# Kernel tuning notes

Measured on AMD Instinct MI355X. Metric: run time of the kernel, lower is better.

## Reference

```python
import jax, jax.numpy as jnp
import numpy as np

B, S, D, H = 4, 2048, 512, 8
DH = D // H  # 64


def setup_inputs() -> dict:
    key = jax.random.key(0)
    ks = jax.random.split(key, 12)
    sc = 0.02
    return {
        "embed": jax.random.normal(ks[0], (B, S, D), dtype=jnp.float32),
        "Wq": jax.random.normal(ks[1], (H, DH, D), dtype=jnp.float32) * sc,
        "bq": jax.random.normal(ks[2], (H, DH), dtype=jnp.float32) * sc,
        "Wk": jax.random.normal(ks[3], (H, DH, D), dtype=jnp.float32) * sc,
        "bk": jax.random.normal(ks[4], (H, DH), dtype=jnp.float32) * sc,
        "Wv": jax.random.normal(ks[5], (H, DH, D), dtype=jnp.float32) * sc,
        "bv": jax.random.normal(ks[6], (H, DH), dtype=jnp.float32) * sc,
        "Wo": jax.random.normal(ks[7], (D, D), dtype=jnp.float32) * sc,
        "bo": jax.random.normal(ks[8], (D,), dtype=jnp.float32) * sc,
        "gamma": jnp.ones((D,), dtype=jnp.float32),
        "beta": jnp.zeros((D,), dtype=jnp.float32),
    }


def reference(embed, Wq, bq, Wk, bk, Wv, bv, Wo, bo, gamma, beta):
    # Per-head linear projections, vectorized over heads: [B,H,S,DH]
    q = jnp.einsum("bsd,hed->bhse", embed, Wq) + bq[None, :, None, :]
    k = jnp.einsum("bsd,hed->bhse", embed, Wk) + bk[None, :, None, :]
    v = jnp.einsum("bsd,hed->bhse", embed, Wv) + bv[None, :, None, :]

    # Full score matrix [B,H,S,S], tril applied to RAW scores (zeros, not -inf),
    # scaled by sqrt(embedding_dim) -- faithful to the original module's math.
    att = jnp.einsum("bhse,bhte->bhst", q, k)
    att = jnp.tril(att)
    att = att / jnp.sqrt(jnp.float32(D))
    att = jax.nn.softmax(att, axis=-1)

    out = jnp.einsum("bhst,bhte->bhse", att, v)  # [B,H,S,DH]
    # concat heads along feature dim -> [B,S,D]
    out = jnp.transpose(out, (0, 2, 1, 3)).reshape(B, S, D)

    x = out @ Wo.T + bo
    x = x + embed

    # LayerNorm over last dim
    mu = jnp.mean(x, axis=-1, keepdims=True)
    var = jnp.var(x, axis=-1, keepdims=True)
    x = (x - mu) / jnp.sqrt(var + 1e-5) * gamma + beta
    return x
```

## Files before the change

kernel.cpp:

```cpp
#include <hip/hip_runtime.h>
#include <hip/hip_bf16.h>


typedef __bf16 bf16;
typedef __bf16 bf16x8 __attribute__((ext_vector_type(8)));
typedef __bf16 bf16x4v __attribute__((ext_vector_type(4)));
typedef float f32x4 __attribute__((ext_vector_type(4)));

#define S_LEN 2048
#define DMODEL 512
#define QSCALE 0.06375870914f

#define GLDS(g, l) __builtin_amdgcn_global_load_lds(                  \
    (const __attribute__((address_space(1))) void*)(g),               \
    (__attribute__((address_space(3))) void*)(l), 16, 0, 0)

__global__ __launch_bounds__(256) void cast_f32_bf16(const float* __restrict__ in,
                                                     bf16* __restrict__ out, int n4) {
  int i = blockIdx.x * blockDim.x + threadIdx.x;
  if (i < n4) {
    float4 v = reinterpret_cast<const float4*>(in)[i];
    bf16x4v o;
    o[0] = (bf16)v.x; o[1] = (bf16)v.y; o[2] = (bf16)v.z; o[3] = (bf16)v.w;
    *reinterpret_cast<bf16x4v*>(out + (size_t)i * 4) = o;
  }
}

__global__ __launch_bounds__(256) void cast4_f32_bf16(
    const float* __restrict__ a0, const float* __restrict__ a1,
    const float* __restrict__ a2, const float* __restrict__ a3,
    bf16* __restrict__ o0, bf16* __restrict__ o1,
    bf16* __restrict__ o2, bf16* __restrict__ o3) {
  int y = blockIdx.y;
  const float* in = (y == 0) ? a0 : (y == 1) ? a1 : (y == 2) ? a2 : a3;
  bf16* out = (y == 0) ? o0 : (y == 1) ? o1 : (y == 2) ? o2 : o3;
  int i = blockIdx.x * blockDim.x + threadIdx.x;
  float4 v = reinterpret_cast<const float4*>(in)[i];
  bf16x4v o;
  o[0] = (bf16)v.x; o[1] = (bf16)v.y; o[2] = (bf16)v.z; o[3] = (bf16)v.w;
  *reinterpret_cast<bf16x4v*>(out + (size_t)i * 4) = o;
}

__device__ __forceinline__ void gemm128_core(
    const bf16* __restrict__ A, const bf16* __restrict__ Bw,
    int row0, int col0, bf16* As, bf16* Bs, f32x4 (&acc)[4][4]) {
  int tid = threadIdx.x;
  int w = tid >> 6, l = tid & 63, lr = l & 15, lg = l >> 4;
  int wr = w >> 1, wc = w & 1;

  int srow = w * 8 + (l >> 3);
  int scol = ((l & 7) ^ (srow & 7)) << 3;
  const bf16* ga = A + (size_t)(row0 + srow) * DMODEL + scol;
  const bf16* gb = Bw + (size_t)(col0 + srow) * DMODEL + scol;
  char* asb = (char*)As;
  char* bsb = (char*)Bs;
  int sbase = w * 1024;

  int aoff[4], boff[4];
#pragma unroll
  for (int m = 0; m < 4; ++m) {
    aoff[m] = (wr * 64 + m * 16 + lr) * 128 + (((lg ^ (lr & 7))) << 4);
    boff[m] = (wc * 64 + m * 16 + lr) * 128 + (((lg ^ (lr & 7))) << 4);
  }

  for (int k0 = 0; k0 < DMODEL; k0 += 64) {
#pragma unroll
    for (int qt = 0; qt < 4; ++qt) {
      GLDS(ga + (size_t)qt * 32 * DMODEL, asb + qt * 4096 + sbase);
      GLDS(gb + (size_t)qt * 32 * DMODEL, bsb + qt * 4096 + sbase);
    }
    ga += 64; gb += 64;
    __syncthreads();

    bf16x8 af[2][4], bfv[2][4];
#pragma unroll
    for (int m = 0; m < 4; ++m) {
      af[0][m] = *(const bf16x8*)(asb + aoff[m]);
      af[1][m] = *(const bf16x8*)(asb + (aoff[m] ^ 0x40));
      bfv[0][m] = *(const bf16x8*)(bsb + boff[m]);
      bfv[1][m] = *(const bf16x8*)(bsb + (boff[m] ^ 0x40));
    }
#pragma unroll
    for (int m = 0; m < 4; ++m)
#pragma unroll
      for (int n = 0; n < 4; ++n) {
        acc[m][n] = __builtin_amdgcn_mfma_f32_16x16x32_bf16(af[0][m], bfv[0][n], acc[m][n], 0, 0, 0);
        acc[m][n] = __builtin_amdgcn_mfma_f32_16x16x32_bf16(af[1][m], bfv[1][n], acc[m][n], 0, 0, 0);
      }
    __syncthreads();
  }
}

__global__ __launch_bounds__(256) void gemm_qkv(
    const bf16* __restrict__ A, const bf16* __restrict__ Wqkv,
    const float* __restrict__ bq, const float* __restrict__ bk, const float* __restrict__ bv,
    bf16* __restrict__ Qb, bf16* __restrict__ Kb, bf16* __restrict__ Vt) {
  __shared__ __align__(16) bf16 As[128 * 64];
  __shared__ __align__(16) bf16 Bs[128 * 64];
  int row0 = blockIdx.x * 128, col0 = blockIdx.y * 128;
  f32x4 acc[4][4] = {};
  gemm128_core(A, Wqkv, row0, col0, As, Bs, acc);

  int tid = threadIdx.x;
  int w = tid >> 6, l = tid & 63, lr = l & 15, lg = l >> 4;
  int wr = w >> 1, wc = w & 1;
  int z2 = col0 >> 9;
  if (z2 < 2) {
    bf16* O = z2 ? Kb : Qb;
    const float* bias = z2 ? bk : bq;
    float qs = z2 ? 1.0f : QSCALE;
#pragma unroll
    for (int n = 0; n < 4; ++n) {
      int cg = (col0 & 511) + wc * 64 + n * 16 + lr;
      float bi = bias[cg];
#pragma unroll
      for (int m = 0; m < 4; ++m) {
        int rg = row0 + wr * 64 + m * 16 + lg * 4;
#pragma unroll
        for (int r = 0; r < 4; ++r)
          O[(size_t)(rg + r) * DMODEL + cg] = (bf16)((acc[m][n][r] + bi) * qs);
      }
    }
  } else {
#pragma unroll
    for (int n = 0; n < 4; ++n) {
      int ep = (col0 & 511) + wc * 64 + n * 16 + lr;
      int h = ep >> 6, e = ep & 63;
      float bi = bv[ep];
#pragma unroll
      for (int m = 0; m < 4; ++m) {
        int rg = row0 + wr * 64 + m * 16 + lg * 4;
        int b = rg >> 11, s0 = rg & 2047;
        bf16x4v pk;
#pragma unroll
        for (int r = 0; r < 4; ++r) pk[r] = (bf16)(acc[m][n][r] + bi);
        *(bf16x4v*)(Vt + ((size_t)((b * 8 + h) * 64 + e)) * S_LEN + s0) = pk;
      }
    }
  }
}

__global__ __launch_bounds__(256) void gemm_wo(
    const bf16* __restrict__ A, const bf16* __restrict__ W,
    const float* __restrict__ bo, const float* __restrict__ embed,
    float* __restrict__ X) {
  __shared__ __align__(16) bf16 As[128 * 64];
  __shared__ __align__(16) bf16 Bs[128 * 64];
  int row0 = blockIdx.x * 128, col0 = blockIdx.y * 128;
  f32x4 acc[4][4] = {};
  gemm128_core(A, W, row0, col0, As, Bs, acc);

  int tid = threadIdx.x;
  int w = tid >> 6, l = tid & 63, lr = l & 15, lg = l >> 4;
  int wr = w >> 1, wc = w & 1;
#pragma unroll
  for (int n = 0; n < 4; ++n) {
    int cg = col0 + wc * 64 + n * 16 + lr;
    float bi = bo[cg];
#pragma unroll
    for (int m = 0; m < 4; ++m) {
      int rg = row0 + wr * 64 + m * 16 + lg * 4;
#pragma unroll
      for (int r = 0; r < 4; ++r)
        X[(size_t)(rg + r) * DMODEL + cg] =
            acc[m][n][r] + bi + embed[(size_t)(rg + r) * DMODEL + cg];
    }
  }
}

__global__ __launch_bounds__(256) void suf_kernel(const bf16* __restrict__ Vt,
                                                  float* __restrict__ SUF) {
  int bh = blockIdx.x;
  int e = threadIdx.x & 63;
  int seg = threadIdx.x >> 6;
  __shared__ float segtot[4][64];
  const bf16* vrow = Vt + ((size_t)bh * 64 + e) * S_LEN;
  float loc[32];
  float carry = 0.f;
#pragma unroll
  for (int j = 31; j >= 0; --j) {
    int jj = seg * 32 + j;
    bf16x8 a = *(const bf16x8*)(vrow + jj * 16);
    bf16x8 b2 = *(const bf16x8*)(vrow + jj * 16 + 8);
    float s = 0.f;
#pragma unroll
    for (int k = 0; k < 8; ++k) s += (float)a[k] + (float)b2[k];
    carry += s;
    loc[j] = carry;
  }
  segtot[seg][e] = carry;
  __syncthreads();
  float add = 0.f;
  for (int s2 = seg + 1; s2 < 4; ++s2) add += segtot[s2][e];
  float* srow = SUF + (size_t)bh * 129 * 64 + e;
#pragma unroll
  for (int j = 0; j < 32; ++j) srow[(size_t)(seg * 32 + j) * 64] = loc[j] + add;
  if (threadIdx.x < 64) srow[(size_t)128 * 64] = 0.f;
}

__global__ __launch_bounds__(512) void flash_attn(
    const bf16* __restrict__ Qb, const bf16* __restrict__ Kb,
    const bf16* __restrict__ Vt, const float* __restrict__ SUF,
    bf16* __restrict__ attO) {
  int bh = blockIdx.y;
  int b = bh >> 3, h = bh & 7;
  int p = (int)gridDim.x - 1 - (int)blockIdx.x;
  int tid = threadIdx.x;
  int w = tid >> 6, l = tid & 63, lr = l & 15, lg = l >> 4;
  int wsub = w & 3;
  int qtile = (w < 4) ? (16 + p) : (15 - p);
  int qb = qtile * 64;
  int nt = 17 + p;

  __shared__ __align__(16) bf16 kl[2][64 * 64];
  __shared__ __align__(16) bf16 vl[2][64 * 64];
  __shared__ __align__(16) bf16 pl[8][16 * 64];

  int srow = qb + 16 * wsub + lr;
  const bf16* qptr = Qb + ((size_t)(b * S_LEN) + srow) * DMODEL + h * 64 + lg * 8;
  bf16x8 aq0 = *(const bf16x8*)(qptr);
  bf16x8 aq1 = *(const bf16x8*)(qptr + 32);

  float lsum[4] = {0.f, 0.f, 0.f, 0.f};
  f32x4 acc[4] = {};

  int tmax_w = qb + 16 * wsub + 16;

  int grow = tid >> 3, gch = tid & 7;
  int sch = ((gch ^ (grow & 7)) << 3);
  const bf16* Kg = Kb + ((size_t)(b * S_LEN) + grow) * DMODEL + h * 64 + sch;
  const bf16* Vg = Vt + ((size_t)(bh * 64) + grow) * S_LEN + sch;
  int sdst = w * 1024;

  int sw0 = (lg ^ (lr & 7)) << 4;
  int sw4 = sw0 ^ 0x40;
  char* plb = (char*)pl[w];

  GLDS(Kg, (char*)kl[0] + sdst);
  GLDS(Vg, (char*)vl[0] + sdst);
  asm volatile("s_waitcnt vmcnt(0)" ::: "memory");
  __syncthreads();

  int cur = 0;
  for (int it = 0; it < nt; ++it) {
    int t0 = it << 6;
    if (it + 1 < nt) {
      GLDS(Kg + (size_t)(t0 + 64) * DMODEL, (char*)kl[cur ^ 1] + sdst);
      GLDS(Vg + (t0 + 64), (char*)vl[cur ^ 1] + sdst);
    }
    if (t0 < tmax_w) {
      char* klb = (char*)kl[cur];
      char* vlb = (char*)vl[cur];

      f32x4 sfrag[4];
      const f32x4 fz = {0.f, 0.f, 0.f, 0.f};
#pragma unroll
      for (int c = 0; c < 4; ++c) {
        int rb = (16 * c + lr) * 128;
        bf16x8 bk0 = *(const bf16x8*)(klb + rb + sw0);
        bf16x8 bk1 = *(const bf16x8*)(klb + rb + sw4);
        f32x4 t = __builtin_amdgcn_mfma_f32_16x16x32_bf16(aq0, bk0, fz, 0, 0, 0);
        sfrag[c] = __builtin_amdgcn_mfma_f32_16x16x32_bf16(aq1, bk1, t, 0, 0, 0);
      }

      if (t0 + 64 <= qb + 16 * wsub) {
#pragma unroll
        for (int r = 0; r < 4; ++r) {
          int row = lg * 4 + r;
          int pbase = row * 128 + ((lr & 7) << 1);
          int xorv = row & 7;
          float psum = 0.f;
#pragma unroll
          for (int c = 0; c < 4; ++c) {
            float pv = exp2f(sfrag[c][r]);
            psum += pv;
            int chunk = 2 * c + (lr >> 3);
            *(bf16*)(plb + pbase + (((chunk ^ xorv) << 4))) = (bf16)pv;
          }
          lsum[r] += psum;
        }
      } else {
#pragma unroll
        for (int r = 0; r < 4; ++r) {
          int sg = qb + 16 * wsub + lg * 4 + r;
          int row = lg * 4 + r;
          int pbase = row * 128 + ((lr & 7) << 1);
          int xorv = row & 7;
          float psum = 0.f;
#pragma unroll
          for (int c = 0; c < 4; ++c) {
            int tg = t0 + 16 * c + lr;
            float x = (tg <= sg) ? sfrag[c][r] : ((tg < tmax_w) ? 0.f : -1e30f);
            float pv = exp2f(x);
            psum += pv;
            int chunk = 2 * c + (lr >> 3);
            *(bf16*)(plb + pbase + (((chunk ^ xorv) << 4))) = (bf16)pv;
          }
          lsum[r] += psum;
        }
      }

      bf16x8 pa0 = *(const bf16x8*)(plb + lr * 128 + sw0);
      bf16x8 pa1 = *(const bf16x8*)(plb + lr * 128 + sw4);
#pragma unroll
      for (int c = 0; c < 4; ++c) {
        int rb = (16 * c + lr) * 128;
        bf16x8 bv0 = *(const bf16x8*)(vlb + rb + sw0);
        bf16x8 bv1 = *(const bf16x8*)(vlb + rb + sw4);
        acc[c] = __builtin_amdgcn_mfma_f32_16x16x32_bf16(pa0, bv0, acc[c], 0, 0, 0);
        acc[c] = __builtin_amdgcn_mfma_f32_16x16x32_bf16(pa1, bv1, acc[c], 0, 0, 0);
      }
    }
    asm volatile("s_waitcnt vmcnt(0)" ::: "memory");
    __syncthreads();
    cur ^= 1;
  }

#pragma unroll
  for (int r = 0; r < 4; ++r) {
#pragma unroll
    for (int d = 1; d < 16; d <<= 1) lsum[r] += __shfl_xor(lsum[r], d, 64);
  }

  int j16 = tmax_w >> 4;
  const float* suf = SUF + ((size_t)bh * 129 + j16) * 64;
  float cnt = (float)(S_LEN - tmax_w);
  float sufe[4];
#pragma unroll
  for (int c = 0; c < 4; ++c) sufe[c] = suf[16 * c + lr];
#pragma unroll
  for (int r = 0; r < 4; ++r) {
    float inv = 1.f / (lsum[r] + cnt);
    int sg = qb + 16 * wsub + lg * 4 + r;
#pragma unroll
    for (int c = 0; c < 4; ++c) {
      float o = (acc[c][r] + sufe[c]) * inv;
      attO[((size_t)(b * S_LEN) + sg) * DMODEL + h * 64 + 16 * c + lr] = (bf16)o;
    }
  }
}

__global__ __launch_bounds__(256) void ln_kernel(const float* __restrict__ x,
                                                 const float* __restrict__ gamma,
                                                 const float* __restrict__ beta,
                                                 float* __restrict__ out) {
  int row = blockIdx.x * 4 + (threadIdx.x >> 6);
  int l = threadIdx.x & 63;
  const float4* xr = reinterpret_cast<const float4*>(x + (size_t)row * DMODEL) + l * 2;
  float4 v0 = xr[0], v1 = xr[1];
  float s = v0.x + v0.y + v0.z + v0.w + v1.x + v1.y + v1.z + v1.w;
  float s2 = v0.x * v0.x + v0.y * v0.y + v0.z * v0.z + v0.w * v0.w +
             v1.x * v1.x + v1.y * v1.y + v1.z * v1.z + v1.w * v1.w;
#pragma unroll
  for (int d = 1; d < 64; d <<= 1) {
    s += __shfl_xor(s, d, 64);
    s2 += __shfl_xor(s2, d, 64);
  }
  float mean = s * (1.f / 512.f);
  float var = s2 * (1.f / 512.f) - mean * mean;
  float rstd = rsqrtf(var + 1e-5f);
  const float4* g4 = reinterpret_cast<const float4*>(gamma) + l * 2;
  const float4* b4 = reinterpret_cast<const float4*>(beta) + l * 2;
  float4 g0 = g4[0], g1 = g4[1], bb0 = b4[0], bb1 = b4[1];
  float4 o0, o1;
  o0.x = (v0.x - mean) * rstd * g0.x + bb0.x;
  o0.y = (v0.y - mean) * rstd * g0.y + bb0.y;
  o0.z = (v0.z - mean) * rstd * g0.z + bb0.z;
  o0.w = (v0.w - mean) * rstd * g0.w + bb0.w;
  o1.x = (v1.x - mean) * rstd * g1.x + bb1.x;
  o1.y = (v1.y - mean) * rstd * g1.y + bb1.y;
  o1.z = (v1.z - mean) * rstd * g1.z + bb1.z;
  o1.w = (v1.w - mean) * rstd * g1.w + bb1.w;
  float4* orow = reinterpret_cast<float4*>(out + (size_t)row * DMODEL) + l * 2;
  orow[0] = o0;
  orow[1] = o1;
}

extern "C" void kernel_launch(void* const* d_in, const int* in_sizes, int n_in,
                              void* d_out, int out_size, void* d_ws, size_t ws_size,
                              hipStream_t stream) {
  const float* embed = (const float*)d_in[0];
  const float* Wq = (const float*)d_in[1];
  const float* bq = (const float*)d_in[2];
  const float* Wk = (const float*)d_in[3];
  const float* bk = (const float*)d_in[4];
  const float* Wv = (const float*)d_in[5];
  const float* bv = (const float*)d_in[6];
  const float* Wo = (const float*)d_in[7];
  const float* bo = (const float*)d_in[8];
  const float* gamma = (const float*)d_in[9];
  const float* beta = (const float*)d_in[10];
  float* out = (float*)d_out;

  char* ws = (char*)d_ws;
  size_t off = 0;
  auto alc = [&](size_t b) { size_t o = off; off += (b + 255) & ~(size_t)255; return o; };
  bf16* Eb    = (bf16*)(ws + alc(8192ull * 512 * 2));
  bf16* Wqkv  = (bf16*)(ws + alc(1536ull * 512 * 2));
  bf16* Wob   = (bf16*)(ws + alc(512ull * 512 * 2));
  bf16* Qb    = (bf16*)(ws + alc(8192ull * 512 * 2));
  bf16* Kb    = (bf16*)(ws + alc(8192ull * 512 * 2));
  bf16* Vt    = (bf16*)(ws + alc(8192ull * 512 * 2));
  float* SUF  = (float*)(ws + alc(32ull * 129 * 64 * 4));
  bf16* AttO  = (bf16*)(ws + alc(8192ull * 512 * 2));
  float* Xb   = (float*)(ws + alc(8192ull * 512 * 4));
  (void)ws_size; (void)n_in; (void)in_sizes; (void)out_size;

  cast_f32_bf16<<<4096, 256, 0, stream>>>(embed, Eb, 4194304 / 4);
  cast4_f32_bf16<<<dim3(256, 4), 256, 0, stream>>>(
      Wq, Wk, Wv, Wo, Wqkv, Wqkv + 512ull * 512, Wqkv + 1024ull * 512, Wob);

  gemm_qkv<<<dim3(64, 12), 256, 0, stream>>>(Eb, Wqkv, bq, bk, bv, Qb, Kb, Vt);
  suf_kernel<<<32, 256, 0, stream>>>(Vt, SUF);
  flash_attn<<<dim3(16, 32), 512, 0, stream>>>(Qb, Kb, Vt, SUF, AttO);
  gemm_wo<<<dim3(64, 4), 256, 0, stream>>>(AttO, Wob, bo, embed, Xb);
  ln_kernel<<<2048, 256, 0, stream>>>(Xb, gamma, beta, out);
}
```

Before: 113.9 us.

## Merge cast kernels, store residual in bf16, widen suffix scan, add MFMA priority

Merges the two cast kernels into one launch, stores the Wo-GEMM plus residual output as bf16 instead of fp32 so the LayerNorm reads half the bytes, and splits the suffix-sum kernel across 8 segments with 512 threads. It also raises wave priority around the MFMA blocks in flash attention. The bf16 intermediate loses precision before LayerNorm. The ideas aim to cut launch overhead and memory traffic in the small kernels.

```diff
diff --git a/kernel.cpp b/kernel.cpp
--- a/kernel.cpp
+++ b/kernel.cpp
@@ -15,30 +15,28 @@
     (const __attribute__((address_space(1))) void*)(g),               \
     (__attribute__((address_space(3))) void*)(l), 16, 0, 0)
 
-__global__ __launch_bounds__(256) void cast_f32_bf16(const float* __restrict__ in,
-                                                     bf16* __restrict__ out, int n4) {
-  int i = blockIdx.x * blockDim.x + threadIdx.x;
-  if (i < n4) {
-    float4 v = reinterpret_cast<const float4*>(in)[i];
-    bf16x4v o;
-    o[0] = (bf16)v.x; o[1] = (bf16)v.y; o[2] = (bf16)v.z; o[3] = (bf16)v.w;
-    *reinterpret_cast<bf16x4v*>(out + (size_t)i * 4) = o;
-  }
-}
-
-__global__ __launch_bounds__(256) void cast4_f32_bf16(
-    const float* __restrict__ a0, const float* __restrict__ a1,
-    const float* __restrict__ a2, const float* __restrict__ a3,
-    bf16* __restrict__ o0, bf16* __restrict__ o1,
-    bf16* __restrict__ o2, bf16* __restrict__ o3) {
-  int y = blockIdx.y;
-  const float* in = (y == 0) ? a0 : (y == 1) ? a1 : (y == 2) ? a2 : a3;
-  bf16* out = (y == 0) ? o0 : (y == 1) ? o1 : (y == 2) ? o2 : o3;
-  int i = blockIdx.x * blockDim.x + threadIdx.x;
-  float4 v = reinterpret_cast<const float4*>(in)[i];
+__global__ __launch_bounds__(256) void cast_all(
+    const float* __restrict__ embed, const float* __restrict__ Wq,
+    const float* __restrict__ Wk, const float* __restrict__ Wv,
+    const float* __restrict__ Wo,
+    bf16* __restrict__ Eb, bf16* __restrict__ Wqkv, bf16* __restrict__ Wob) {
+  int i = blockIdx.x * 256 + threadIdx.x;
+  const float* src;
+  bf16* dst;
+  int il;
+  if (i < 1048576) {
+    src = embed; dst = Eb; il = i;
+  } else {
+    int j = i - 1048576;
+    int w = j >> 16;
+    il = j & 65535;
+    src = (w == 0) ? Wq : (w == 1) ? Wk : (w == 2) ? Wv : Wo;
+    dst = (w == 3) ? Wob : Wqkv + (size_t)w * 262144;
+  }
+  float4 v = reinterpret_cast<const float4*>(src)[il];
   bf16x4v o;
   o[0] = (bf16)v.x; o[1] = (bf16)v.y; o[2] = (bf16)v.z; o[3] = (bf16)v.w;
-  *reinterpret_cast<bf16x4v*>(out + (size_t)i * 4) = o;
+  *reinterpret_cast<bf16x4v*>(dst + (size_t)il * 4) = o;
 }
 
 __device__ __forceinline__ void gemm128_core(
@@ -143,7 +141,7 @@
 __global__ __launch_bounds__(256) void gemm_wo(
     const bf16* __restrict__ A, const bf16* __restrict__ W,
     const float* __restrict__ bo, const float* __restrict__ embed,
-    float* __restrict__ X) {
+    bf16* __restrict__ X) {
   __shared__ __align__(16) bf16 As[128 * 64];
   __shared__ __align__(16) bf16 Bs[128 * 64];
   int row0 = blockIdx.x * 128, col0 = blockIdx.y * 128;
@@ -163,23 +161,23 @@
 #pragma unroll
       for (int r = 0; r < 4; ++r)
         X[(size_t)(rg + r) * DMODEL + cg] =
-            acc[m][n][r] + bi + embed[(size_t)(rg + r) * DMODEL + cg];
-    }
-  }
-}
-
-__global__ __launch_bounds__(256) void suf_kernel(const bf16* __restrict__ Vt,
+            (bf16)(acc[m][n][r] + bi + embed[(size_t)(rg + r) * DMODEL + cg]);
+    }
+  }
+}
+
+__global__ __launch_bounds__(512) void suf_kernel(const bf16* __restrict__ Vt,
                                                   float* __restrict__ SUF) {
   int bh = blockIdx.x;
   int e = threadIdx.x & 63;
   int seg = threadIdx.x >> 6;
-  __shared__ float segtot[4][64];
+  __shared__ float segtot[8][64];
   const bf16* vrow = Vt + ((size_t)bh * 64 + e) * S_LEN;
-  float loc[32];
+  float loc[16];
   float carry = 0.f;
 #pragma unroll
-  for (int j = 31; j >= 0; --j) {
-    int jj = seg * 32 + j;
+  for (int j = 15; j >= 0; --j) {
+    int jj = seg * 16 + j;
     bf16x8 a = *(const bf16x8*)(vrow + jj * 16);
     bf16x8 b2 = *(const bf16x8*)(vrow + jj * 16 + 8);
     float s = 0.f;
@@ -191,10 +189,10 @@
   segtot[seg][e] = carry;
   __syncthreads();
   float add = 0.f;
-  for (int s2 = seg + 1; s2 < 4; ++s2) add += segtot[s2][e];
+  for (int s2 = seg + 1; s2 < 8; ++s2) add += segtot[s2][e];
   float* srow = SUF + (size_t)bh * 129 * 64 + e;
 #pragma unroll
-  for (int j = 0; j < 32; ++j) srow[(size_t)(seg * 32 + j) * 64] = loc[j] + add;
+  for (int j = 0; j < 16; ++j) srow[(size_t)(seg * 16 + j) * 64] = loc[j] + add;
   if (threadIdx.x < 64) srow[(size_t)128 * 64] = 0.f;
 }
 
@@ -254,6 +252,7 @@
 
       f32x4 sfrag[4];
       const f32x4 fz = {0.f, 0.f, 0.f, 0.f};
+      __builtin_amdgcn_s_setprio(1);
 #pragma unroll
       for (int c = 0; c < 4; ++c) {
         int rb = (16 * c + lr) * 128;
@@ -262,6 +261,7 @@
         f32x4 t = __builtin_amdgcn_mfma_f32_16x16x32_bf16(aq0, bk0, fz, 0, 0, 0);
         sfrag[c] = __builtin_amdgcn_mfma_f32_16x16x32_bf16(aq1, bk1, t, 0, 0, 0);
       }
+      __builtin_amdgcn_s_setprio(0);
 
       if (t0 + 64 <= qb + 16 * wsub) {
 #pragma unroll
@@ -302,6 +302,7 @@
 
       bf16x8 pa0 = *(const bf16x8*)(plb + lr * 128 + sw0);
       bf16x8 pa1 = *(const bf16x8*)(plb + lr * 128 + sw4);
+      __builtin_amdgcn_s_setprio(1);
 #pragma unroll
       for (int c = 0; c < 4; ++c) {
         int rb = (16 * c + lr) * 128;
@@ -310,6 +311,7 @@
         acc[c] = __builtin_amdgcn_mfma_f32_16x16x32_bf16(pa0, bv0, acc[c], 0, 0, 0);
         acc[c] = __builtin_amdgcn_mfma_f32_16x16x32_bf16(pa1, bv1, acc[c], 0, 0, 0);
       }
+      __builtin_amdgcn_s_setprio(0);
     }
     asm volatile("s_waitcnt vmcnt(0)" ::: "memory");
     __syncthreads();
@@ -340,17 +342,21 @@
   }
 }
 
-__global__ __launch_bounds__(256) void ln_kernel(const float* __restrict__ x,
+__global__ __launch_bounds__(256) void ln_kernel(const bf16* __restrict__ x,
                                                  const float* __restrict__ gamma,
                                                  const float* __restrict__ beta,
                                                  float* __restrict__ out) {
   int row = blockIdx.x * 4 + (threadIdx.x >> 6);
   int l = threadIdx.x & 63;
-  const float4* xr = reinterpret_cast<const float4*>(x + (size_t)row * DMODEL) + l * 2;
-  float4 v0 = xr[0], v1 = xr[1];
-  float s = v0.x + v0.y + v0.z + v0.w + v1.x + v1.y + v1.z + v1.w;
-  float s2 = v0.x * v0.x + v0.y * v0.y + v0.z * v0.z + v0.w * v0.w +
-             v1.x * v1.x + v1.y * v1.y + v1.z * v1.z + v1.w * v1.w;
+  bf16x8 xv = *(const bf16x8*)(x + (size_t)row * DMODEL + l * 8);
+  float xf[8];
+  float s = 0.f, s2 = 0.f;
+#pragma unroll
+  for (int k = 0; k < 8; ++k) {
+    xf[k] = (float)xv[k];
+    s += xf[k];
+    s2 += xf[k] * xf[k];
+  }
 #pragma unroll
   for (int d = 1; d < 64; d <<= 1) {
     s += __shfl_xor(s, d, 64);
@@ -363,14 +369,14 @@
   const float4* b4 = reinterpret_cast<const float4*>(beta) + l * 2;
   float4 g0 = g4[0], g1 = g4[1], bb0 = b4[0], bb1 = b4[1];
   float4 o0, o1;
-  o0.x = (v0.x - mean) * rstd * g0.x + bb0.x;
-  o0.y = (v0.y - mean) * rstd * g0.y + bb0.y;
-  o0.z = (v0.z - mean) * rstd * g0.z + bb0.z;
-  o0.w = (v0.w - mean) * rstd * g0.w + bb0.w;
-  o1.x = (v1.x - mean) * rstd * g1.x + bb1.x;
-  o1.y = (v1.y - mean) * rstd * g1.y + bb1.y;
-  o1.z = (v1.z - mean) * rstd * g1.z + bb1.z;
-  o1.w = (v1.w - mean) * rstd * g1.w + bb1.w;
+  o0.x = (xf[0] - mean) * rstd * g0.x + bb0.x;
+  o0.y = (xf[1] - mean) * rstd * g0.y + bb0.y;
+  o0.z = (xf[2] - mean) * rstd * g0.z + bb0.z;
+  o0.w = (xf[3] - mean) * rstd * g0.w + bb0.w;
+  o1.x = (xf[4] - mean) * rstd * g1.x + bb1.x;
+  o1.y = (xf[5] - mean) * rstd * g1.y + bb1.y;
+  o1.z = (xf[6] - mean) * rstd * g1.z + bb1.z;
+  o1.w = (xf[7] - mean) * rstd * g1.w + bb1.w;
   float4* orow = reinterpret_cast<float4*>(out + (size_t)row * DMODEL) + l * 2;
   orow[0] = o0;
   orow[1] = o1;
@@ -403,15 +409,13 @@
   bf16* Vt    = (bf16*)(ws + alc(8192ull * 512 * 2));
   float* SUF  = (float*)(ws + alc(32ull * 129 * 64 * 4));
   bf16* AttO  = (bf16*)(ws + alc(8192ull * 512 * 2));
-  float* Xb   = (float*)(ws + alc(8192ull * 512 * 4));
+  bf16* Xb    = (bf16*)(ws + alc(8192ull * 512 * 2));
   (void)ws_size; (void)n_in; (void)in_sizes; (void)out_size;
 
-  cast_f32_bf16<<<4096, 256, 0, stream>>>(embed, Eb, 4194304 / 4);
-  cast4_f32_bf16<<<dim3(256, 4), 256, 0, stream>>>(
-      Wq, Wk, Wv, Wo, Wqkv, Wqkv + 512ull * 512, Wqkv + 1024ull * 512, Wob);
+  cast_all<<<5120, 256, 0, stream>>>(embed, Wq, Wk, Wv, Wo, Eb, Wqkv, Wob);
 
   gemm_qkv<<<dim3(64, 12), 256, 0, stream>>>(Eb, Wqkv, bq, bk, bv, Qb, Kb, Vt);
-  suf_kernel<<<32, 256, 0, stream>>>(Vt, SUF);
+  suf_kernel<<<32, 512, 0, stream>>>(Vt, SUF);
   flash_attn<<<dim3(16, 32), 512, 0, stream>>>(Qb, Kb, Vt, SUF, AttO);
   gemm_wo<<<dim3(64, 4), 256, 0, stream>>>(AttO, Wob, bo, embed, Xb);
   ln_kernel<<<2048, 256, 0, stream>>>(Xb, gamma, beta, out);
```

Result: faster. 111.3 us (-2.3%).
